# Kernel optimization log

Hardware: AMD Instinct MI355X
Metric: run time of the kernel (lower is better)

The kernel has to match this reference:

```python
import jax, jax.numpy as jnp
import numpy as np

H = 1024
NH = 16
HD = H // NH
EPS = 1e-5


def _layernorm(x, g, b):
    mu = jnp.mean(x, axis=-1, keepdims=True)
    var = jnp.mean((x - mu) ** 2, axis=-1, keepdims=True)
    return (x - mu) * jax.lax.rsqrt(var + EPS) * g + b


def setup_inputs() -> dict:
    key = jax.random.key(0)
    ks = jax.random.split(key, 12)
    s = lambda fan_in: 1.0 / np.sqrt(fan_in)
    x = jax.random.normal(ks[0], (2, 2048, H), dtype=jnp.float32)
    return {
        "x": x,
        "ln1_g": jnp.ones((H,), jnp.float32),
        "ln1_b": jnp.zeros((H,), jnp.float32),
        "W_qkv": jax.random.uniform(ks[1], (H, 3 * H), jnp.float32, -s(H), s(H)),
        "b_qkv": jax.random.uniform(ks[2], (3 * H,), jnp.float32, -s(H), s(H)),
        "W_out": jax.random.uniform(ks[3], (H, H), jnp.float32, -s(H), s(H)),
        "b_out": jax.random.uniform(ks[4], (H,), jnp.float32, -s(H), s(H)),
        "ln2_g": jnp.ones((H,), jnp.float32),
        "ln2_b": jnp.zeros((H,), jnp.float32),
        "W1": jax.random.uniform(ks[5], (H, 4 * H), jnp.float32, -s(H), s(H)),
        "b1": jax.random.uniform(ks[6], (4 * H,), jnp.float32, -s(H), s(H)),
        "W2": jax.random.uniform(ks[7], (4 * H, H), jnp.float32, -s(4 * H), s(4 * H)),
        "b2": jax.random.uniform(ks[8], (H,), jnp.float32, -s(4 * H), s(4 * H)),
    }


def reference(x, ln1_g, ln1_b, W_qkv, b_qkv, W_out, b_out, ln2_g, ln2_b, W1, b1, W2, b2):
    B, S, _ = x.shape
    residual = x
    h = _layernorm(x, ln1_g, ln1_b)
    qkv = h @ W_qkv + b_qkv                     # [B,S,3H]
    qkv = qkv.reshape(B, S, 3, NH, HD)
    q, k, v = qkv[:, :, 0], qkv[:, :, 1], qkv[:, :, 2]  # [B,S,NH,HD]
    scale = 1.0 / np.sqrt(HD)
    attn = jnp.einsum("bqhd,bkhd->bhqk", q, k) * scale  # [B,NH,S,S]
    attn = jax.nn.softmax(attn, axis=-1)
    out = jnp.einsum("bhqk,bkhd->bqhd", attn, v).reshape(B, S, H)
    x = residual + (out @ W_out + b_out)
    residual = x
    h = _layernorm(x, ln2_g, ln2_b)
    h = jax.nn.gelu(h @ W1 + b1, approximate=False) @ W2 + b2
    return residual + h
```

## Files before the change

kernel.cpp:

```cpp
#include <hip/hip_runtime.h>
#include <hip/hip_bf16.h>
#include <math.h>

#define HDIM 1024
#define SEQ  2048
#define BATCH 2
#define NHEAD 16
#define HEADD 64

typedef short bf16x8 __attribute__((ext_vector_type(8)));
typedef float f32x4  __attribute__((ext_vector_type(4)));
typedef unsigned short u16x8 __attribute__((ext_vector_type(8)));

__device__ __forceinline__ unsigned short f2bf(float f) {
    unsigned u = __float_as_uint(f);
    unsigned r = (u + 0x7FFFu + ((u >> 16) & 1u)) >> 16;
    return (unsigned short)r;
}
__device__ __forceinline__ float b2f(unsigned short s) {
    return __uint_as_float(((unsigned)s) << 16);
}
__device__ __forceinline__ unsigned pk2bf(float lo, float hi) {
    __hip_bfloat162 h = __float22bfloat162_rn(float2{lo, hi});
    unsigned r;
    __builtin_memcpy(&r, &h, 4);
    return r;
}
__device__ __forceinline__ float fexp2(float x) {
#if __has_builtin(__builtin_amdgcn_exp2f)
    return __builtin_amdgcn_exp2f(x);
#else
    return exp2f(x);
#endif
}
__device__ __forceinline__ void gld16(void* lds, const void* g) {
    __builtin_amdgcn_global_load_lds(
        (const __attribute__((address_space(1))) unsigned int*)(g),
        (__attribute__((address_space(3))) unsigned int*)(lds),
        16, 0, 0);
}

#define SWZ(row, chunk) (((row) * 64) + (((chunk) ^ ((row) & 7)) << 3))

__global__ __launch_bounds__(256) void ln_kernel(const float* __restrict__ x,
                                                 const float* __restrict__ gw,
                                                 const float* __restrict__ bw,
                                                 unsigned short* __restrict__ y)
{
    int row = blockIdx.x;
    int t = threadIdx.x;
    const float* xr = x + (size_t)row * HDIM;
    float4 v = *(const float4*)(xr + t * 4);
    float s1 = v.x + v.y + v.z + v.w;
    float s2 = v.x * v.x + v.y * v.y + v.z * v.z + v.w * v.w;
#pragma unroll
    for (int m = 1; m < 64; m <<= 1) {
        s1 += __shfl_xor(s1, m);
        s2 += __shfl_xor(s2, m);
    }
    __shared__ float red[8];
    int wid = t >> 6;
    if ((t & 63) == 0) { red[wid * 2] = s1; red[wid * 2 + 1] = s2; }
    __syncthreads();
    if (t == 0) {
        float a = red[0] + red[2] + red[4] + red[6];
        float b = red[1] + red[3] + red[5] + red[7];
        red[0] = a; red[1] = b;
    }
    __syncthreads();
    float mu  = red[0] * (1.0f / HDIM);
    float var = red[1] * (1.0f / HDIM) - mu * mu;
    float rs  = rsqrtf(var + 1e-5f);
    float4 g4 = *(const float4*)(gw + t * 4);
    float4 b4 = *(const float4*)(bw + t * 4);
    ushort4 o;
    o.x = f2bf((v.x - mu) * rs * g4.x + b4.x);
    o.y = f2bf((v.y - mu) * rs * g4.y + b4.y);
    o.z = f2bf((v.z - mu) * rs * g4.z + b4.z);
    o.w = f2bf((v.w - mu) * rs * g4.w + b4.w);
    *(ushort4*)(y + (size_t)row * HDIM + t * 4) = o;
}

__global__ __launch_bounds__(256) void wconv_kernel(const float* __restrict__ W,
                                                    unsigned short* __restrict__ WT,
                                                    int K, int N)
{
    __shared__ float tile[32][33];
    int n0 = blockIdx.x * 32, k0 = blockIdx.y * 32;
    int t = threadIdx.x, c = t & 31, r = t >> 5;
#pragma unroll
    for (int i = 0; i < 4; ++i)
        tile[r + 8 * i][c] = W[(size_t)(k0 + r + 8 * i) * N + n0 + c];
    __syncthreads();
#pragma unroll
    for (int i = 0; i < 4; ++i)
        WT[(size_t)(n0 + r + 8 * i) * K + k0 + c] = f2bf(tile[c][r + 8 * i]);
}

template <int EPI>
__global__ __launch_bounds__(256, 2) void mgemm(const unsigned short* __restrict__ A,
                                                const unsigned short* __restrict__ BT,
                                                const float* __restrict__ bias,
                                                const float* __restrict__ resid,
                                                float* __restrict__ Cf,
                                                unsigned short* __restrict__ Cb,
                                                int M, int N, int K)
{
    __shared__ char smem[65536];
    int t = threadIdx.x;
    int bn = blockIdx.x * 128, bm = blockIdx.y * 128;
    int l = t & 63, w = t >> 6;
    int wm = w >> 1, wn = w & 1;
    int lrow = l & 15, kq = l >> 4;

    f32x4 acc[4][4];
#pragma unroll
    for (int i = 0; i < 4; ++i)
#pragma unroll
        for (int j = 0; j < 4; ++j) acc[i][j] = {0.f, 0.f, 0.f, 0.f};

    const unsigned short* Ap[4];
    const unsigned short* Bp[4];
    int ld[4];
#pragma unroll
    for (int i = 0; i < 4; ++i) {
        int cid = i * 256 + t;
        int row = cid >> 3, c = cid & 7;
        int gc = (c ^ (row & 7)) << 3;
        Ap[i] = A + (size_t)(bm + row) * K + gc;
        Bp[i] = BT + (size_t)(bn + row) * K + gc;
        ld[i] = cid << 4;
    }

    int nt = K >> 6;
#pragma unroll
    for (int i = 0; i < 4; ++i) {
        gld16(smem + ld[i], Ap[i]);
        gld16(smem + 16384 + ld[i], Bp[i]);
    }
    __syncthreads();

    for (int tk = 0; tk < nt; ++tk) {
        int cur = (tk & 1) << 15;
        if (tk + 1 < nt) {
            int k0 = (tk + 1) << 6;
            int nxt = 32768 - cur;
#pragma unroll
            for (int i = 0; i < 4; ++i) {
                gld16(smem + nxt + ld[i], Ap[i] + k0);
                gld16(smem + nxt + 16384 + ld[i], Bp[i] + k0);
            }
        }
        const unsigned short* sA = (const unsigned short*)(smem + cur);
        const unsigned short* sB = (const unsigned short*)(smem + cur + 16384);
#pragma unroll
        for (int kk = 0; kk < 2; ++kk) {
            bf16x8 af[4], bv[4];
#pragma unroll
            for (int mi = 0; mi < 4; ++mi)
                af[mi] = *(const bf16x8*)(sA + SWZ(wm * 64 + mi * 16 + lrow, kk * 4 + kq));
#pragma unroll
            for (int ni = 0; ni < 4; ++ni)
                bv[ni] = *(const bf16x8*)(sB + SWZ(wn * 64 + ni * 16 + lrow, kk * 4 + kq));
#pragma unroll
            for (int mi = 0; mi < 4; ++mi)
#pragma unroll
                for (int ni = 0; ni < 4; ++ni)
                    acc[mi][ni] = __builtin_amdgcn_mfma_f32_16x16x32_bf16(af[mi], bv[ni], acc[mi][ni], 0, 0, 0);
        }
        __syncthreads();
    }

    int crow = (l >> 4) * 4;
    int ccol = l & 15;
#pragma unroll
    for (int mi = 0; mi < 4; ++mi) {
#pragma unroll
        for (int ni = 0; ni < 4; ++ni) {
            int gcol = bn + wn * 64 + ni * 16 + ccol;
            float bv = bias[gcol];
#pragma unroll
            for (int r = 0; r < 4; ++r) {
                int grow = bm + wm * 64 + mi * 16 + crow + r;
                size_t off = (size_t)grow * N + gcol;
                float v = acc[mi][ni][r] + bv;
                if (EPI == 1) {
                    Cf[off] = v + resid[off];
                } else if (EPI == 2) {
                    v = 0.5f * v * (1.0f + erff(v * 0.70710678118654752f));
                    Cb[off] = f2bf(v);
                } else {
                    Cb[off] = f2bf(v);
                }
            }
        }
    }
}

__global__ __launch_bounds__(256) void mattn(const unsigned short* __restrict__ qkv,
                                             unsigned short* __restrict__ out)
{
    __shared__ unsigned short Qs[64 * 64];
    __shared__ unsigned short Ks[64 * 64];
    __shared__ unsigned short Vt[64 * 64];
    __shared__ unsigned short Ps[4 * 16 * 64];
    int t = threadIdx.x;
    int w = t >> 6, l = t & 63;
    int lr = l & 15, lh = l >> 4;
    int q0 = blockIdx.x * 64;
    int hh = blockIdx.y, b = blockIdx.z;
    const unsigned short* Qg = qkv + (size_t)b * SEQ * 3072 + hh * 64;
    const unsigned short* Kg = Qg + 1024;
    const unsigned short* Vg = Qg + 2048;

#pragma unroll
    for (int i = 0; i < 2; ++i) {
        int chunkid = (w * 2 + i) * 64 + l;
        int row = chunkid >> 3, c = chunkid & 7;
        gld16(((char*)Qs) + chunkid * 16,
              Qg + (size_t)(q0 + row) * 3072 + ((c ^ (row & 7)) << 3));
    }
    __syncthreads();
    bf16x8 qa[2];
#pragma unroll
    for (int ks = 0; ks < 2; ++ks)
        qa[ks] = *(const bf16x8*)(Qs + SWZ(w * 16 + lr, ks * 4 + lh));

    f32x4 o[4];
#pragma unroll
    for (int i = 0; i < 4; ++i) o[i] = {0.f, 0.f, 0.f, 0.f};
    float mr = -3.0e38f, lsum = 0.f;
    unsigned short* Pw = Ps + w * (16 * 64);
    const float C = 0.18033688011112042f;

    int ck0 = (w * 2) * 64 + l, ck1 = (w * 2 + 1) * 64 + l;
    int kr0 = ck0 >> 3, kc0 = ck0 & 7;
    int kr1 = ck1 >> 3, kc1 = ck1 & 7;
    const unsigned short* Kp0 = Kg + (size_t)kr0 * 3072 + ((kc0 ^ (kr0 & 7)) << 3);
    const unsigned short* Kp1 = Kg + (size_t)kr1 * 3072 + ((kc1 ^ (kr1 & 7)) << 3);
    char* Kd0 = (char*)Ks + ck0 * 16;
    char* Kd1 = (char*)Ks + ck1 * 16;
    int vk = (t & 31) * 2;
    int vd0 = ((t >> 5) & 7) * 8;
    const unsigned short* Vp0 = Vg + (size_t)vk * 3072 + vd0;
    const unsigned short* Vp1 = Vp0 + 3072;

    for (int kv = 0; kv < SEQ; kv += 64) {
        __syncthreads();
        gld16(Kd0, Kp0);
        gld16(Kd1, Kp1);
        u16x8 v0 = *(const u16x8*)Vp0;
        u16x8 v1 = *(const u16x8*)Vp1;
        Kp0 += 64 * 3072; Kp1 += 64 * 3072;
        Vp0 += 64 * 3072; Vp1 += 64 * 3072;
#pragma unroll
        for (int j = 0; j < 8; ++j) {
            int d = vd0 + j;
            unsigned pack = (unsigned)(unsigned short)v0[j] | ((unsigned)(unsigned short)v1[j] << 16);
            *(unsigned*)(Vt + SWZ(d, vk >> 3) + (vk & 7)) = pack;
        }
        __syncthreads();

        f32x4 s[4];
#pragma unroll
        for (int ni = 0; ni < 4; ++ni) s[ni] = {0.f, 0.f, 0.f, 0.f};
#pragma unroll
        for (int ks = 0; ks < 2; ++ks) {
#pragma unroll
            for (int ni = 0; ni < 4; ++ni) {
                bf16x8 kb = *(const bf16x8*)(Ks + SWZ(ni * 16 + lr, ks * 4 + lh));
                s[ni] = __builtin_amdgcn_mfma_f32_16x16x32_bf16(kb, qa[ks], s[ni], 0, 0, 0);
            }
        }
        float mx = s[0][0];
#pragma unroll
        for (int ni = 0; ni < 4; ++ni)
#pragma unroll
            for (int r = 0; r < 4; ++r) mx = fmaxf(mx, s[ni][r]);
        mx = fmaxf(mx, __shfl_xor(mx, 16));
        mx = fmaxf(mx, __shfl_xor(mx, 32));
        if (__any(mx > mr + 64.0f)) {
            float mn = fmaxf(mr, mx);
            float corr = fexp2((mr - mn) * C);
            mr = mn;
            lsum *= corr;
            float cr[4];
#pragma unroll
            for (int r = 0; r < 4; ++r) cr[r] = __shfl(corr, lh * 4 + r, 16);
#pragma unroll
            for (int nd = 0; nd < 4; ++nd) {
                o[nd][0] *= cr[0]; o[nd][1] *= cr[1];
                o[nd][2] *= cr[2]; o[nd][3] *= cr[3];
            }
        }
        float mc = mr * C;
        float rsum = 0.f;
#pragma unroll
        for (int ni = 0; ni < 4; ++ni)
#pragma unroll
            for (int r = 0; r < 4; ++r) {
                float p = fexp2(fmaf(s[ni][r], C, -mc));
                s[ni][r] = p;
                rsum += p;
            }
        rsum += __shfl_xor(rsum, 16);
        rsum += __shfl_xor(rsum, 32);
        lsum += rsum;
#pragma unroll
        for (int ni = 0; ni < 4; ++ni)
#pragma unroll
            for (int rp = 0; rp < 2; ++rp) {
                int k = ni * 16 + lh * 4 + rp * 2;
                *(unsigned*)(Pw + SWZ(lr, k >> 3) + (k & 7)) =
                    pk2bf(s[ni][rp * 2], s[ni][rp * 2 + 1]);
            }
#pragma unroll
        for (int ks = 0; ks < 2; ++ks) {
            bf16x8 pa = *(const bf16x8*)(Pw + SWZ(lr, ks * 4 + lh));
#pragma unroll
            for (int nd = 0; nd < 4; ++nd) {
                bf16x8 vb = *(const bf16x8*)(Vt + SWZ(nd * 16 + lr, ks * 4 + lh));
                o[nd] = __builtin_amdgcn_mfma_f32_16x16x32_bf16(pa, vb, o[nd], 0, 0, 0);
            }
        }
    }
    float inv = 1.0f / lsum;
    float ir[4];
#pragma unroll
    for (int r = 0; r < 4; ++r) ir[r] = __shfl(inv, lh * 4 + r, 16);
#pragma unroll
    for (int r = 0; r < 4; ++r) {
        int q = q0 + w * 16 + lh * 4 + r;
#pragma unroll
        for (int nd = 0; nd < 4; ++nd) {
            int d = nd * 16 + lr;
            out[(size_t)((size_t)b * SEQ + q) * HDIM + hh * 64 + d] = f2bf(o[nd][r] * ir[r]);
        }
    }
}

extern "C" void kernel_launch(void* const* d_in, const int* in_sizes, int n_in,
                              void* d_out, int out_size, void* d_ws, size_t ws_size,
                              hipStream_t stream)
{
    const float* x     = (const float*)d_in[0];
    const float* ln1_g = (const float*)d_in[1];
    const float* ln1_b = (const float*)d_in[2];
    const float* W_qkv = (const float*)d_in[3];
    const float* b_qkv = (const float*)d_in[4];
    const float* W_out = (const float*)d_in[5];
    const float* b_out = (const float*)d_in[6];
    const float* ln2_g = (const float*)d_in[7];
    const float* ln2_b = (const float*)d_in[8];
    const float* W1    = (const float*)d_in[9];
    const float* b1    = (const float*)d_in[10];
    const float* W2    = (const float*)d_in[11];
    const float* b2    = (const float*)d_in[12];
    float* out = (float*)d_out;
    char* ws8  = (char*)d_ws;

    const int M = BATCH * SEQ;
    const size_t MB = 1048576;

    unsigned short* hbuf = (unsigned short*)(ws8);
    unsigned short* qkvb = (unsigned short*)(ws8 + 8 * MB);
    unsigned short* attb = (unsigned short*)(ws8 + 32 * MB);
    unsigned short* ffn1 = (unsigned short*)(ws8 + 8 * MB);
    unsigned short* WqT  = (unsigned short*)(ws8 + 40 * MB);
    unsigned short* WoT  = (unsigned short*)(ws8 + 46 * MB);
    unsigned short* W1T  = (unsigned short*)(ws8 + 48 * MB);
    unsigned short* W2T  = (unsigned short*)(ws8 + 56 * MB);

    wconv_kernel<<<dim3(3 * HDIM / 32, HDIM / 32), 256, 0, stream>>>(W_qkv, WqT, HDIM, 3 * HDIM);
    wconv_kernel<<<dim3(HDIM / 32, HDIM / 32), 256, 0, stream>>>(W_out, WoT, HDIM, HDIM);
    wconv_kernel<<<dim3(4 * HDIM / 32, HDIM / 32), 256, 0, stream>>>(W1, W1T, HDIM, 4 * HDIM);
    wconv_kernel<<<dim3(HDIM / 32, 4 * HDIM / 32), 256, 0, stream>>>(W2, W2T, 4 * HDIM, HDIM);

    ln_kernel<<<M, 256, 0, stream>>>(x, ln1_g, ln1_b, hbuf);
    mgemm<0><<<dim3(3 * HDIM / 128, M / 128), 256, 0, stream>>>(hbuf, WqT, b_qkv, nullptr, nullptr, qkvb, M, 3 * HDIM, HDIM);
    mattn<<<dim3(SEQ / 64, NHEAD, BATCH), 256, 0, stream>>>(qkvb, attb);
    mgemm<1><<<dim3(HDIM / 128, M / 128), 256, 0, stream>>>(attb, WoT, b_out, x, out, nullptr, M, HDIM, HDIM);
    ln_kernel<<<M, 256, 0, stream>>>(out, ln2_g, ln2_b, hbuf);
    mgemm<2><<<dim3(4 * HDIM / 128, M / 128), 256, 0, stream>>>(hbuf, W1T, b1, nullptr, nullptr, ffn1, M, 4 * HDIM, HDIM);
    mgemm<1><<<dim3(HDIM / 128, M / 128), 256, 0, stream>>>(ffn1, W2T, b2, out, out, nullptr, M, HDIM, 4 * HDIM);
}
```

Measured before the change: 254.1 us.

## Use 256x128 GEMM tiles with triple-buffered LDS, split-K atomics for residual GEMMs

Replaces the 128x128 GEMM with a 512-thread 256x128 tile kernel that uses a three-stage LDS ring fed by direct global-to-LDS loads, partial vmcnt waits and raised MFMA priority. The two residual-add GEMMs (out-proj and FFN2) now use split-K=2 and accumulate with float atomicAdd into an output buffer pre-seeded with x by the first layernorm kernel. This aims to cut global-memory latency stalls, improve operand reuse, and fill the GPU for the narrow N=1024 GEMMs. In exchange it uses 144KB of LDS per block, adds atomic traffic, and makes the fp32 summation order nondeterministic.

```diff
diff --git a/kernel.cpp b/kernel.cpp
--- a/kernel.cpp
+++ b/kernel.cpp
@@ -45,12 +45,14 @@
 __global__ __launch_bounds__(256) void ln_kernel(const float* __restrict__ x,
                                                  const float* __restrict__ gw,
                                                  const float* __restrict__ bw,
-                                                 unsigned short* __restrict__ y)
+                                                 unsigned short* __restrict__ y,
+                                                 float* __restrict__ xcopy)
 {
     int row = blockIdx.x;
     int t = threadIdx.x;
     const float* xr = x + (size_t)row * HDIM;
     float4 v = *(const float4*)(xr + t * 4);
+    if (xcopy) *(float4*)(xcopy + (size_t)row * HDIM + t * 4) = v;
     float s1 = v.x + v.y + v.z + v.w;
     float s2 = v.x * v.x + v.y * v.y + v.z * v.z + v.w * v.w;
 #pragma unroll
@@ -97,21 +99,22 @@
         WT[(size_t)(n0 + r + 8 * i) * K + k0 + c] = f2bf(tile[c][r + 8 * i]);
 }
 
-template <int EPI>
-__global__ __launch_bounds__(256, 2) void mgemm(const unsigned short* __restrict__ A,
-                                                const unsigned short* __restrict__ BT,
-                                                const float* __restrict__ bias,
-                                                const float* __restrict__ resid,
-                                                float* __restrict__ Cf,
-                                                unsigned short* __restrict__ Cb,
-                                                int M, int N, int K)
+template <int EPI, int SPLITK>
+__global__ __launch_bounds__(512, 2) void mgemm3(const unsigned short* __restrict__ A,
+                                                 const unsigned short* __restrict__ BT,
+                                                 const float* __restrict__ bias,
+                                                 float* __restrict__ Cf,
+                                                 unsigned short* __restrict__ Cb,
+                                                 int M, int N, int K)
 {
-    __shared__ char smem[65536];
+    __shared__ char smem[147456];
     int t = threadIdx.x;
-    int bn = blockIdx.x * 128, bm = blockIdx.y * 128;
+    int bn = blockIdx.x * 128, bm = blockIdx.y * 256;
+    int Ks = K / SPLITK;
+    int kbase = blockIdx.z * Ks;
     int l = t & 63, w = t >> 6;
     int wm = w >> 1, wn = w & 1;
-    int lrow = l & 15, kq = l >> 4;
+    int lr = l & 15, kq = l >> 4;
 
     f32x4 acc[4][4];
 #pragma unroll
@@ -119,56 +122,69 @@
 #pragma unroll
         for (int j = 0; j < 4; ++j) acc[i][j] = {0.f, 0.f, 0.f, 0.f};
 
-    const unsigned short* Ap[4];
-    const unsigned short* Bp[4];
-    int ld[4];
-#pragma unroll
-    for (int i = 0; i < 4; ++i) {
-        int cid = i * 256 + t;
-        int row = cid >> 3, c = cid & 7;
-        int gc = (c ^ (row & 7)) << 3;
-        Ap[i] = A + (size_t)(bm + row) * K + gc;
-        Bp[i] = BT + (size_t)(bn + row) * K + gc;
-        ld[i] = cid << 4;
-    }
-
-    int nt = K >> 6;
-#pragma unroll
-    for (int i = 0; i < 4; ++i) {
-        gld16(smem + ld[i], Ap[i]);
-        gld16(smem + 16384 + ld[i], Bp[i]);
-    }
-    __syncthreads();
-
+    const unsigned short* gsrc[6];
+    int ldst[6];
+#pragma unroll
+    for (int i = 0; i < 6; ++i) {
+        int cid = i * 512 + t;
+        if (cid < 2048) {
+            int row = cid >> 3, c = cid & 7;
+            gsrc[i] = A + (size_t)(bm + row) * K + kbase + ((c ^ (row & 7)) << 3);
+            ldst[i] = cid << 4;
+        } else {
+            int bc = cid - 2048;
+            int row = bc >> 3, c = bc & 7;
+            gsrc[i] = BT + (size_t)(bn + row) * K + kbase + ((c ^ (row & 7)) << 3);
+            ldst[i] = 32768 + (bc << 4);
+        }
+    }
+
+    int nt = Ks >> 6;
+#pragma unroll
+    for (int s = 0; s < 2; ++s)
+#pragma unroll
+        for (int i = 0; i < 6; ++i)
+            gld16(smem + s * 49152 + ldst[i], gsrc[i] + (size_t)s * 64);
+    asm volatile("s_waitcnt vmcnt(6)" ::: "memory");
+    __builtin_amdgcn_s_barrier();
+
+    int cur = 0;
     for (int tk = 0; tk < nt; ++tk) {
-        int cur = (tk & 1) << 15;
-        if (tk + 1 < nt) {
-            int k0 = (tk + 1) << 6;
-            int nxt = 32768 - cur;
-#pragma unroll
-            for (int i = 0; i < 4; ++i) {
-                gld16(smem + nxt + ld[i], Ap[i] + k0);
-                gld16(smem + nxt + 16384 + ld[i], Bp[i] + k0);
-            }
-        }
-        const unsigned short* sA = (const unsigned short*)(smem + cur);
-        const unsigned short* sB = (const unsigned short*)(smem + cur + 16384);
+        if (tk + 2 < nt) {
+            int sb = cur - 1; if (sb < 0) sb = 2;
+            size_t koff = (size_t)(tk + 2) * 64;
+#pragma unroll
+            for (int i = 0; i < 6; ++i)
+                gld16(smem + sb * 49152 + ldst[i], gsrc[i] + koff);
+        }
+        const unsigned short* sA = (const unsigned short*)(smem + cur * 49152);
+        const unsigned short* sB = (const unsigned short*)(smem + cur * 49152 + 32768);
 #pragma unroll
         for (int kk = 0; kk < 2; ++kk) {
             bf16x8 af[4], bv[4];
 #pragma unroll
             for (int mi = 0; mi < 4; ++mi)
-                af[mi] = *(const bf16x8*)(sA + SWZ(wm * 64 + mi * 16 + lrow, kk * 4 + kq));
+                af[mi] = *(const bf16x8*)(sA + SWZ(wm * 64 + mi * 16 + lr, kk * 4 + kq));
 #pragma unroll
             for (int ni = 0; ni < 4; ++ni)
-                bv[ni] = *(const bf16x8*)(sB + SWZ(wn * 64 + ni * 16 + lrow, kk * 4 + kq));
+                bv[ni] = *(const bf16x8*)(sB + SWZ(wn * 64 + ni * 16 + lr, kk * 4 + kq));
+            __builtin_amdgcn_s_setprio(1);
 #pragma unroll
             for (int mi = 0; mi < 4; ++mi)
 #pragma unroll
                 for (int ni = 0; ni < 4; ++ni)
                     acc[mi][ni] = __builtin_amdgcn_mfma_f32_16x16x32_bf16(af[mi], bv[ni], acc[mi][ni], 0, 0, 0);
-        }
-        __syncthreads();
+            __builtin_amdgcn_s_setprio(0);
+        }
+        if (tk + 1 < nt) {
+            if (tk + 2 < nt) {
+                asm volatile("s_waitcnt vmcnt(6)" ::: "memory");
+            } else {
+                asm volatile("s_waitcnt vmcnt(0)" ::: "memory");
+            }
+            __builtin_amdgcn_s_barrier();
+        }
+        cur = cur + 1; if (cur == 3) cur = 0;
     }
 
     int crow = (l >> 4) * 4;
@@ -183,14 +199,16 @@
             for (int r = 0; r < 4; ++r) {
                 int grow = bm + wm * 64 + mi * 16 + crow + r;
                 size_t off = (size_t)grow * N + gcol;
-                float v = acc[mi][ni][r] + bv;
-                if (EPI == 1) {
-                    Cf[off] = v + resid[off];
+                float v = acc[mi][ni][r];
+                if (EPI == 0) {
+                    Cb[off] = f2bf(v + bv);
                 } else if (EPI == 2) {
+                    v += bv;
                     v = 0.5f * v * (1.0f + erff(v * 0.70710678118654752f));
                     Cb[off] = f2bf(v);
                 } else {
-                    Cb[off] = f2bf(v);
+                    if (blockIdx.z == 0) v += bv;
+                    atomicAdd(Cf + off, v);
                 }
             }
         }
@@ -376,11 +394,11 @@
     wconv_kernel<<<dim3(4 * HDIM / 32, HDIM / 32), 256, 0, stream>>>(W1, W1T, HDIM, 4 * HDIM);
     wconv_kernel<<<dim3(HDIM / 32, 4 * HDIM / 32), 256, 0, stream>>>(W2, W2T, 4 * HDIM, HDIM);
 
-    ln_kernel<<<M, 256, 0, stream>>>(x, ln1_g, ln1_b, hbuf);
-    mgemm<0><<<dim3(3 * HDIM / 128, M / 128), 256, 0, stream>>>(hbuf, WqT, b_qkv, nullptr, nullptr, qkvb, M, 3 * HDIM, HDIM);
+    ln_kernel<<<M, 256, 0, stream>>>(x, ln1_g, ln1_b, hbuf, out);
+    mgemm3<0, 1><<<dim3(3 * HDIM / 128, M / 256, 1), 512, 0, stream>>>(hbuf, WqT, b_qkv, nullptr, qkvb, M, 3 * HDIM, HDIM);
     mattn<<<dim3(SEQ / 64, NHEAD, BATCH), 256, 0, stream>>>(qkvb, attb);
-    mgemm<1><<<dim3(HDIM / 128, M / 128), 256, 0, stream>>>(attb, WoT, b_out, x, out, nullptr, M, HDIM, HDIM);
-    ln_kernel<<<M, 256, 0, stream>>>(out, ln2_g, ln2_b, hbuf);
-    mgemm<2><<<dim3(4 * HDIM / 128, M / 128), 256, 0, stream>>>(hbuf, W1T, b1, nullptr, nullptr, ffn1, M, 4 * HDIM, HDIM);
-    mgemm<1><<<dim3(HDIM / 128, M / 128), 256, 0, stream>>>(ffn1, W2T, b2, out, out, nullptr, M, HDIM, 4 * HDIM);
-}
+    mgemm3<3, 2><<<dim3(HDIM / 128, M / 256, 2), 512, 0, stream>>>(attb, WoT, b_out, out, nullptr, M, HDIM, HDIM);
+    ln_kernel<<<M, 256, 0, stream>>>(out, ln2_g, ln2_b, hbuf, nullptr);
+    mgemm3<2, 1><<<dim3(4 * HDIM / 128, M / 256, 1), 512, 0, stream>>>(hbuf, W1T, b1, nullptr, ffn1, M, 4 * HDIM, HDIM);
+    mgemm3<3, 2><<<dim3(HDIM / 128, M / 256, 2), 512, 0, stream>>>(ffn1, W2T, b2, out, nullptr, M, HDIM, 4 * HDIM);
+}
```

Result: slower. 295.2 us (+16.2%).

## Add 256x256-tile 512-thread GEMM for QKV and FFN1 projections

Applied to the files above, without the earlier changes.

Introduces a larger-tile MFMA GEMM kernel with 256x256 output tiles, 8 waves, and a double-buffered 128 KB LDS staging area with swizzled layout. The QKV and first FFN projections now use it instead of the 128x128 kernel. The aim is to raise operand reuse per LDS load and cut global traffic per FLOP. The cost is one block per CU with heavy register and LDS use, and fewer blocks, which can leave CUs underused on the QKV grid.

```diff
diff --git a/kernel.cpp b/kernel.cpp
--- a/kernel.cpp
+++ b/kernel.cpp
@@ -187,6 +187,104 @@
                 if (EPI == 1) {
                     Cf[off] = v + resid[off];
                 } else if (EPI == 2) {
+                    v = 0.5f * v * (1.0f + erff(v * 0.70710678118654752f));
+                    Cb[off] = f2bf(v);
+                } else {
+                    Cb[off] = f2bf(v);
+                }
+            }
+        }
+    }
+}
+
+template <int EPI>
+__global__ __launch_bounds__(512, 1) void mgemm256(const unsigned short* __restrict__ A,
+                                                   const unsigned short* __restrict__ BT,
+                                                   const float* __restrict__ bias,
+                                                   float* __restrict__ Cf,
+                                                   unsigned short* __restrict__ Cb,
+                                                   int M, int N, int K)
+{
+    __shared__ char smem[131072];
+    int t = threadIdx.x;
+    int bn = blockIdx.x * 256, bm = blockIdx.y * 256;
+    int l = t & 63, w = t >> 6;
+    int wm = w >> 2, wn = w & 3;
+    int lr = l & 15, kq = l >> 4;
+
+    f32x4 acc[8][4];
+#pragma unroll
+    for (int i = 0; i < 8; ++i)
+#pragma unroll
+        for (int j = 0; j < 4; ++j) acc[i][j] = {0.f, 0.f, 0.f, 0.f};
+
+    const unsigned short* Ap[4];
+    const unsigned short* Bp[4];
+    int ld[4];
+#pragma unroll
+    for (int i = 0; i < 4; ++i) {
+        int cid = i * 512 + t;
+        int row = cid >> 3, c = cid & 7;
+        int gc = (c ^ (row & 7)) << 3;
+        Ap[i] = A + (size_t)(bm + row) * K + gc;
+        Bp[i] = BT + (size_t)(bn + row) * K + gc;
+        ld[i] = cid << 4;
+    }
+
+    int nt = K >> 6;
+#pragma unroll
+    for (int i = 0; i < 4; ++i) {
+        gld16(smem + ld[i], Ap[i]);
+        gld16(smem + 32768 + ld[i], Bp[i]);
+    }
+    __syncthreads();
+
+    for (int tk = 0; tk < nt; ++tk) {
+        int cur = (tk & 1) << 16;
+        if (tk + 1 < nt) {
+            int k0 = (tk + 1) << 6;
+            int nxt = 65536 - cur;
+#pragma unroll
+            for (int i = 0; i < 4; ++i) {
+                gld16(smem + nxt + ld[i], Ap[i] + k0);
+                gld16(smem + nxt + 32768 + ld[i], Bp[i] + k0);
+            }
+        }
+        const unsigned short* sA = (const unsigned short*)(smem + cur);
+        const unsigned short* sB = (const unsigned short*)(smem + cur + 32768);
+#pragma unroll
+        for (int kk = 0; kk < 2; ++kk) {
+            bf16x8 bv[4];
+#pragma unroll
+            for (int ni = 0; ni < 4; ++ni)
+                bv[ni] = *(const bf16x8*)(sB + SWZ(wn * 64 + ni * 16 + lr, kk * 4 + kq));
+            __builtin_amdgcn_s_setprio(1);
+#pragma unroll
+            for (int mi = 0; mi < 8; ++mi) {
+                bf16x8 af = *(const bf16x8*)(sA + SWZ(wm * 128 + mi * 16 + lr, kk * 4 + kq));
+#pragma unroll
+                for (int ni = 0; ni < 4; ++ni)
+                    acc[mi][ni] = __builtin_amdgcn_mfma_f32_16x16x32_bf16(af, bv[ni], acc[mi][ni], 0, 0, 0);
+            }
+            __builtin_amdgcn_s_setprio(0);
+        }
+        __syncthreads();
+    }
+
+    int crow = (l >> 4) * 4;
+    int ccol = l & 15;
+#pragma unroll
+    for (int mi = 0; mi < 8; ++mi) {
+#pragma unroll
+        for (int ni = 0; ni < 4; ++ni) {
+            int gcol = bn + wn * 64 + ni * 16 + ccol;
+            float bv = bias[gcol];
+#pragma unroll
+            for (int r = 0; r < 4; ++r) {
+                int grow = bm + wm * 128 + mi * 16 + crow + r;
+                size_t off = (size_t)grow * N + gcol;
+                float v = acc[mi][ni][r] + bv;
+                if (EPI == 2) {
                     v = 0.5f * v * (1.0f + erff(v * 0.70710678118654752f));
                     Cb[off] = f2bf(v);
                 } else {
@@ -377,10 +475,10 @@
     wconv_kernel<<<dim3(HDIM / 32, 4 * HDIM / 32), 256, 0, stream>>>(W2, W2T, 4 * HDIM, HDIM);
 
     ln_kernel<<<M, 256, 0, stream>>>(x, ln1_g, ln1_b, hbuf);
-    mgemm<0><<<dim3(3 * HDIM / 128, M / 128), 256, 0, stream>>>(hbuf, WqT, b_qkv, nullptr, nullptr, qkvb, M, 3 * HDIM, HDIM);
+    mgemm256<0><<<dim3(3 * HDIM / 256, M / 256), 512, 0, stream>>>(hbuf, WqT, b_qkv, nullptr, qkvb, M, 3 * HDIM, HDIM);
     mattn<<<dim3(SEQ / 64, NHEAD, BATCH), 256, 0, stream>>>(qkvb, attb);
     mgemm<1><<<dim3(HDIM / 128, M / 128), 256, 0, stream>>>(attb, WoT, b_out, x, out, nullptr, M, HDIM, HDIM);
     ln_kernel<<<M, 256, 0, stream>>>(out, ln2_g, ln2_b, hbuf);
-    mgemm<2><<<dim3(4 * HDIM / 128, M / 128), 256, 0, stream>>>(hbuf, W1T, b1, nullptr, nullptr, ffn1, M, 4 * HDIM, HDIM);
+    mgemm256<2><<<dim3(4 * HDIM / 256, M / 256), 512, 0, stream>>>(hbuf, W1T, b1, nullptr, ffn1, M, 4 * HDIM, HDIM);
     mgemm<1><<<dim3(HDIM / 128, M / 128), 256, 0, stream>>>(ffn1, W2T, b2, out, out, nullptr, M, HDIM, 4 * HDIM);
 }
```

New measurement: 274.7 us. +8.1%, slower.

## Double-buffer K/V tiles in attention with register prefetch of the next tile

Applied to the files above, without the earlier changes.

The attention kernel now keeps two LDS buffers for K and V. The next tile is prefetched from global memory into registers while the current tile is computed, then written into the alternate buffer, so each iteration needs one barrier instead of two. This aims to hide global load latency behind the MFMA and softmax work. In exchange it doubles LDS use for K/V, which may reduce occupancy, and adds register pressure from holding the prefetched tile.

```diff
diff --git a/kernel.cpp b/kernel.cpp
--- a/kernel.cpp
+++ b/kernel.cpp
@@ -201,8 +201,8 @@
                                              unsigned short* __restrict__ out)
 {
     __shared__ unsigned short Qs[64 * 64];
-    __shared__ unsigned short Ks[64 * 64];
-    __shared__ unsigned short Vt[64 * 64];
+    __shared__ unsigned short Ks[2][64 * 64];
+    __shared__ unsigned short Vt[2][64 * 64];
     __shared__ unsigned short Ps[4 * 16 * 64];
     int t = threadIdx.x;
     int w = t >> 6, l = t & 63;
@@ -220,11 +220,43 @@
         gld16(((char*)Qs) + chunkid * 16,
               Qg + (size_t)(q0 + row) * 3072 + ((c ^ (row & 7)) << 3));
     }
+
+    int kr0 = t >> 3, kc0 = t & 7;
+    int kr1 = (t + 256) >> 3;
+    const unsigned short* Kp0 = Kg + (size_t)kr0 * 3072 + kc0 * 8;
+    const unsigned short* Kp1 = Kg + (size_t)kr1 * 3072 + kc0 * 8;
+    int kd0 = SWZ(kr0, kc0);
+    int kd1 = SWZ(kr1, kc0);
+    int vk = (t & 31) * 2;
+    int vd0 = ((t >> 5) & 7) * 8;
+    const unsigned short* Vp0 = Vg + (size_t)vk * 3072 + vd0;
+    const unsigned short* Vp1 = Vp0 + 3072;
+
+    u16x8 k0 = *(const u16x8*)Kp0;
+    u16x8 k1 = *(const u16x8*)Kp1;
+    u16x8 v0 = *(const u16x8*)Vp0;
+    u16x8 v1 = *(const u16x8*)Vp1;
+    Kp0 += 64 * 3072; Kp1 += 64 * 3072; Vp0 += 64 * 3072; Vp1 += 64 * 3072;
+
     __syncthreads();
     bf16x8 qa[2];
 #pragma unroll
     for (int ks = 0; ks < 2; ++ks)
         qa[ks] = *(const bf16x8*)(Qs + SWZ(w * 16 + lr, ks * 4 + lh));
+
+    *(u16x8*)(Ks[0] + kd0) = k0;
+    *(u16x8*)(Ks[0] + kd1) = k1;
+#pragma unroll
+    for (int j = 0; j < 8; ++j) {
+        int d = vd0 + j;
+        unsigned pack = (unsigned)(unsigned short)v0[j] | ((unsigned)(unsigned short)v1[j] << 16);
+        *(unsigned*)(Vt[0] + SWZ(d, vk >> 3) + (vk & 7)) = pack;
+    }
+    k0 = *(const u16x8*)Kp0; k1 = *(const u16x8*)Kp1;
+    v0 = *(const u16x8*)Vp0; v1 = *(const u16x8*)Vp1;
+    Kp0 += 64 * 3072; Kp1 += 64 * 3072; Vp0 += 64 * 3072; Vp1 += 64 * 3072;
+    asm volatile("s_waitcnt lgkmcnt(0)" ::: "memory");
+    __builtin_amdgcn_s_barrier();
 
     f32x4 o[4];
 #pragma unroll
@@ -233,33 +265,10 @@
     unsigned short* Pw = Ps + w * (16 * 64);
     const float C = 0.18033688011112042f;
 
-    int ck0 = (w * 2) * 64 + l, ck1 = (w * 2 + 1) * 64 + l;
-    int kr0 = ck0 >> 3, kc0 = ck0 & 7;
-    int kr1 = ck1 >> 3, kc1 = ck1 & 7;
-    const unsigned short* Kp0 = Kg + (size_t)kr0 * 3072 + ((kc0 ^ (kr0 & 7)) << 3);
-    const unsigned short* Kp1 = Kg + (size_t)kr1 * 3072 + ((kc1 ^ (kr1 & 7)) << 3);
-    char* Kd0 = (char*)Ks + ck0 * 16;
-    char* Kd1 = (char*)Ks + ck1 * 16;
-    int vk = (t & 31) * 2;
-    int vd0 = ((t >> 5) & 7) * 8;
-    const unsigned short* Vp0 = Vg + (size_t)vk * 3072 + vd0;
-    const unsigned short* Vp1 = Vp0 + 3072;
-
-    for (int kv = 0; kv < SEQ; kv += 64) {
-        __syncthreads();
-        gld16(Kd0, Kp0);
-        gld16(Kd1, Kp1);
-        u16x8 v0 = *(const u16x8*)Vp0;
-        u16x8 v1 = *(const u16x8*)Vp1;
-        Kp0 += 64 * 3072; Kp1 += 64 * 3072;
-        Vp0 += 64 * 3072; Vp1 += 64 * 3072;
-#pragma unroll
-        for (int j = 0; j < 8; ++j) {
-            int d = vd0 + j;
-            unsigned pack = (unsigned)(unsigned short)v0[j] | ((unsigned)(unsigned short)v1[j] << 16);
-            *(unsigned*)(Vt + SWZ(d, vk >> 3) + (vk & 7)) = pack;
-        }
-        __syncthreads();
+    const int nt = SEQ / 64;
+    for (int tt = 0; tt < nt; ++tt) {
+        const unsigned short* Kc = Ks[tt & 1];
+        const unsigned short* Vc = Vt[tt & 1];
 
         f32x4 s[4];
 #pragma unroll
@@ -268,7 +277,7 @@
         for (int ks = 0; ks < 2; ++ks) {
 #pragma unroll
             for (int ni = 0; ni < 4; ++ni) {
-                bf16x8 kb = *(const bf16x8*)(Ks + SWZ(ni * 16 + lr, ks * 4 + lh));
+                bf16x8 kb = *(const bf16x8*)(Kc + SWZ(ni * 16 + lr, ks * 4 + lh));
                 s[ni] = __builtin_amdgcn_mfma_f32_16x16x32_bf16(kb, qa[ks], s[ni], 0, 0, 0);
             }
         }
@@ -319,9 +328,28 @@
             bf16x8 pa = *(const bf16x8*)(Pw + SWZ(lr, ks * 4 + lh));
 #pragma unroll
             for (int nd = 0; nd < 4; ++nd) {
-                bf16x8 vb = *(const bf16x8*)(Vt + SWZ(nd * 16 + lr, ks * 4 + lh));
+                bf16x8 vb = *(const bf16x8*)(Vc + SWZ(nd * 16 + lr, ks * 4 + lh));
                 o[nd] = __builtin_amdgcn_mfma_f32_16x16x32_bf16(pa, vb, o[nd], 0, 0, 0);
             }
+        }
+
+        if (tt + 1 < nt) {
+            int nb = (tt & 1) ^ 1;
+            *(u16x8*)(Ks[nb] + kd0) = k0;
+            *(u16x8*)(Ks[nb] + kd1) = k1;
+#pragma unroll
+            for (int j = 0; j < 8; ++j) {
+                int d = vd0 + j;
+                unsigned pack = (unsigned)(unsigned short)v0[j] | ((unsigned)(unsigned short)v1[j] << 16);
+                *(unsigned*)(Vt[nb] + SWZ(d, vk >> 3) + (vk & 7)) = pack;
+            }
+            if (tt + 2 < nt) {
+                k0 = *(const u16x8*)Kp0; k1 = *(const u16x8*)Kp1;
+                v0 = *(const u16x8*)Vp0; v1 = *(const u16x8*)Vp1;
+                Kp0 += 64 * 3072; Kp1 += 64 * 3072; Vp0 += 64 * 3072; Vp1 += 64 * 3072;
+            }
+            asm volatile("s_waitcnt lgkmcnt(0)" ::: "memory");
+            __builtin_amdgcn_s_barrier();
         }
     }
     float inv = 1.0f / lsum;
```

After: 255.1 us. About the same (+0.4%).
